# Performance work log

Hardware: AMD Instinct MI355X
Metric: run time of the kernel (lower is better)

## Reference

```python
import jax, jax.numpy as jnp
import numpy as np

N = 200_000
E = 6_400_000
EPS = 1e-12


def l2_normalize(x):
    # F.normalize(x, p=2, dim=1): x / max(||x||_2, eps)
    n = jnp.linalg.norm(x, axis=1, keepdims=True)
    return x / jnp.maximum(n, EPS)


def gcn_conv(x, W, b, src, dst, n):
    """PyG GCNConv: add self-loops, symmetric normalization D^-1/2 A D^-1/2,
    linear transform (no bias) on nodes, scatter-add to targets, then + bias."""
    loop = jnp.arange(n)
    s = jnp.concatenate([src, loop])  # sources (messages gathered here)
    d = jnp.concatenate([dst, loop])  # targets (aggregation here)
    deg = jax.ops.segment_sum(jnp.ones(s.shape[0], dtype=x.dtype), d, num_segments=n)
    dinv = jnp.where(deg > 0, jax.lax.rsqrt(deg), 0.0)
    norm = dinv[s] * dinv[d]  # [E+N]
    h = x @ W  # [N, out]
    out = jax.ops.segment_sum(norm[:, None] * h[s], d, num_segments=n)
    return out + b


def setup_inputs() -> dict:
    key = jax.random.key(0)
    ks = jax.random.split(key, 10)
    x = jax.random.normal(ks[0], (N, 3), dtype=jnp.float32)
    edge_index = jax.random.randint(ks[1], (2, E), 0, N, dtype=jnp.int64)

    def glorot(k, shape):
        lim = float(np.sqrt(6.0 / (shape[0] + shape[1])))
        return jax.random.uniform(k, shape, jnp.float32, -lim, lim)

    return {
        "x": x,
        "edge_index": edge_index,
        "W1": glorot(ks[2], (3, 6)),   "b1": jnp.zeros((6,), jnp.float32),
        "W2": glorot(ks[3], (6, 12)),  "b2": jnp.zeros((12,), jnp.float32),
        "W3": glorot(ks[4], (12, 24)), "b3": jnp.zeros((24,), jnp.float32),
        "Wc": glorot(ks[5], (24, 13)), "bc": jnp.zeros((13,), jnp.float32),
    }


def reference(x, edge_index, W1, b1, W2, b2, W3, b3, Wc, bc):
    src, dst = edge_index[0], edge_index[1]
    n = x.shape[0]
    h = jnp.tanh(gcn_conv(x, W1, b1, src, dst, n))
    h = jnp.tanh(l2_normalize(gcn_conv(h, W2, b2, src, dst, n)))
    h = l2_normalize(gcn_conv(h, W3, b3, src, dst, n))
    h = h @ Wc + bc
    return l2_normalize(h)
```

## Files before the change

### kernel.cpp

```cpp
#include <hip/hip_runtime.h>
#include <math.h>


static constexpr int NN = 200000;
static constexpr int NE = 6400000;
static constexpr int BK = 256;

static constexpr int SUBW  = 512;
static constexpr int NBA   = (NN + SUBW - 1) / SUBW;
static constexpr int CAP   = 32;
static constexpr int FLUSH = 16;
static constexpr int CAPB  = 18400;
static constexpr int BKP   = 512;
static constexpr int EPT   = 4;
static constexpr int CHUNK = BKP * EPT;
static constexpr int GPART = 768;
static constexpr int SRCSH = 13;
static constexpr int NSB   = (NN + (1 << SRCSH) - 1) >> SRCSH;

static constexpr int S     = 4;
static constexpr int LOGS  = 2;

__global__ void __launch_bounds__(BKP) k_part(const int* __restrict__ srcI,
                                              const int* __restrict__ dstI,
                                              unsigned* __restrict__ stg,
                                              int* __restrict__ gtail, int e) {
  __shared__ unsigned bin[CAP][NBA];
  __shared__ int bcnt[NBA];
  for (int t = threadIdx.x; t < NBA; t += BKP) bcnt[t] = 0;
  __syncthreads();
  int nchunks = (e + CHUNK - 1) / CHUNK;
  for (int c = blockIdx.x; c < nchunks; c += gridDim.x) {
    int base_i = c * CHUNK;
    int dv[EPT], sv[EPT];
#pragma unroll
    for (int u = 0; u < EPT; ++u) {
      int i = base_i + u * BKP + (int)threadIdx.x;
      dv[u] = (i < e) ? __builtin_nontemporal_load(dstI + i) : -1;
      sv[u] = (i < e) ? __builtin_nontemporal_load(srcI + i) : 0;
    }
#pragma unroll
    for (int u = 0; u < EPT; ++u) {
      if (dv[u] >= 0) {
        int b = dv[u] >> 9;
        unsigned rec = ((unsigned)(dv[u] & (SUBW - 1)) << 18) | (unsigned)sv[u];
        int p = atomicAdd(&bcnt[b], 1);
        if (p < CAP) {
          bin[p][b] = rec;
        } else {
          int base = atomicAdd(&gtail[b], 1);
          stg[(size_t)b * CAPB + base] = rec;
        }
      }
    }
    __syncthreads();
    int b2 = threadIdx.x;
    if (b2 < NBA) {
      int c2 = bcnt[b2];
      if (c2 > CAP) c2 = CAP;
      if (c2 >= FLUSH) {
        int nfl = c2 & ~(FLUSH - 1);
        int base = atomicAdd(&gtail[b2], nfl);
        size_t o = (size_t)b2 * CAPB + base;
        for (int k = 0; k < nfl; k += 4) {
          uint4 v;
          v.x = bin[k][b2]; v.y = bin[k + 1][b2]; v.z = bin[k + 2][b2]; v.w = bin[k + 3][b2];
          *(uint4*)(stg + o + k) = v;
        }
        int r = c2 - nfl;
        for (int k = 0; k < r; ++k) bin[k][b2] = bin[nfl + k][b2];
        bcnt[b2] = r;
      }
    }
    __syncthreads();
  }
  int b2 = threadIdx.x;
  if (b2 < NBA) {
    int c2 = bcnt[b2];
    if (c2 > CAP) c2 = CAP;
    if (c2 > 0) {
      int base = atomicAdd(&gtail[b2], c2);
      size_t o = (size_t)b2 * CAPB + base;
      for (int k = 0; k < c2; ++k) stg[o + k] = bin[k][b2];
    }
  }
}

__global__ void k_scan_sub(const int* __restrict__ gtail, int* __restrict__ sbase) {
  __shared__ int s0[512], s1[512];
  int t = threadIdx.x;
  int v = (t < NBA) ? gtail[t] : 0;
  s0[t] = v;
  __syncthreads();
  int* a = s0; int* b = s1;
  for (int off = 1; off < 512; off <<= 1) {
    int x = a[t] + ((t >= off) ? a[t - off] : 0);
    b[t] = x;
    __syncthreads();
    int* tmp = a; a = b; b = tmp;
  }
  if (t < NBA) sbase[t] = a[t] - v;
}

__global__ void __launch_bounds__(BK) k_build(const unsigned* __restrict__ stg,
                                              const int* __restrict__ gtail,
                                              const int* __restrict__ sbase,
                                              int* __restrict__ rowptr,
                                              int* __restrict__ adj) {
  __shared__ unsigned hist2[SUBW * NSB];
  __shared__ int htot[SUBW];
  __shared__ int s0[SUBW], s1[SUBW];
  int b = blockIdx.x;
  int m = gtail[b]; if (m > CAPB) m = CAPB;
  size_t off = (size_t)b * CAPB;
  int base = sbase[b];
  if (b == NBA - 1 && threadIdx.x == 0) rowptr[NN] = base + m;
  for (int t = threadIdx.x; t < SUBW * NSB; t += BK) hist2[t] = 0;
  __syncthreads();
  for (int k = threadIdx.x; k < m; k += BK) {
    unsigned rec = stg[off + k];
    int dl = rec >> 18;
    int sb = (int)((rec & 0x3FFFFu) >> SRCSH);
    atomicAdd(&hist2[dl * NSB + sb], 1u);
  }
  __syncthreads();
  for (int dl = threadIdx.x; dl < SUBW; dl += BK) {
    unsigned run = 0;
    for (int sb = 0; sb < NSB; ++sb) {
      unsigned c = hist2[dl * NSB + sb];
      hist2[dl * NSB + sb] = run;
      run += c;
    }
    htot[dl] = (int)run;
    s0[dl] = (int)run;
  }
  __syncthreads();
  int* a = s0; int* bb = s1;
  for (int o2 = 1; o2 < SUBW; o2 <<= 1) {
    for (int t = threadIdx.x; t < SUBW; t += BK) bb[t] = a[t] + ((t >= o2) ? a[t - o2] : 0);
    __syncthreads();
    int* tmp = a; a = bb; bb = tmp;
  }
  for (int t = threadIdx.x; t < SUBW; t += BK) {
    int node = b * SUBW + t;
    int ex = a[t] - htot[t];
    if (node < NN) rowptr[node] = base + ex;
    bb[t] = ex;
  }
  __syncthreads();
  for (int k = threadIdx.x; k < m; k += BK) {
    unsigned rec = stg[off + k];
    int dl = rec >> 18;
    unsigned src = rec & 0x3FFFFu;
    int sb = (int)(src >> SRCSH);
    int p = bb[dl] + (int)atomicAdd(&hist2[dl * NSB + sb], 1u);
    adj[base + p] = (int)src;
  }
}

__global__ void k_zero(int* __restrict__ p, int n) {
  int i = blockIdx.x * blockDim.x + threadIdx.x;
  if (i < n) p[i] = 0;
}

__global__ void k_dinv(const int* __restrict__ rowptr, float* __restrict__ dinv, int n) {
  int i = blockIdx.x * blockDim.x + threadIdx.x;
  if (i < n) dinv[i] = rsqrtf(1.0f + (float)(rowptr[i + 1] - rowptr[i]));
}

__global__ void k_prep(const float* __restrict__ x, const float* __restrict__ dinv,
                       float* __restrict__ p1, int n) {
  int i = blockIdx.x * blockDim.x + threadIdx.x;
  if (i >= n) return;
  float di = dinv[i];
  float3 v;
  v.x = di * x[3 * (size_t)i];
  v.y = di * x[3 * (size_t)i + 1];
  v.z = di * x[3 * (size_t)i + 2];
  *(float3*)(p1 + 3 * (size_t)i) = v;
}

template <int RW> struct RowT;
template <> struct RowT<3> {
  using T = float3;
  static __device__ inline T ld(const float* __restrict__ p) { return *(const float3*)p; }
  static __device__ inline void add(float* __restrict__ a, const T& v) {
    a[0] += v.x; a[1] += v.y; a[2] += v.z;
  }
};
template <> struct RowT<6> {
  struct T { float2 a, b, c; };
  static __device__ inline T ld(const float* __restrict__ p) {
    T t; t.a = *(const float2*)p; t.b = *(const float2*)(p + 2); t.c = *(const float2*)(p + 4);
    return t;
  }
  static __device__ inline void add(float* __restrict__ a, const T& v) {
    a[0] += v.a.x; a[1] += v.a.y; a[2] += v.b.x; a[3] += v.b.y; a[4] += v.c.x; a[5] += v.c.y;
  }
};
template <> struct RowT<12> {
  struct T { float4 a, b, c; };
  static __device__ inline T ld(const float* __restrict__ p) {
    T t; t.a = *(const float4*)p; t.b = *(const float4*)(p + 4); t.c = *(const float4*)(p + 8);
    return t;
  }
  static __device__ inline void add(float* __restrict__ a, const T& v) {
    a[0] += v.a.x; a[1] += v.a.y; a[2] += v.a.z; a[3] += v.a.w;
    a[4] += v.b.x; a[5] += v.b.y; a[6] += v.b.z; a[7] += v.b.w;
    a[8] += v.c.x; a[9] += v.c.y; a[10] += v.c.z; a[11] += v.c.w;
  }
};

template <int RW, int UN>
__device__ inline void gather_p(const int* __restrict__ adj, int st, int en,
                                const float* __restrict__ pin, float* __restrict__ acc,
                                int slot) {
  using RT = RowT<RW>;
  using T = typename RT::T;
  int k = st + slot;
  if (k + (UN - 1) * S < en) {
    int a[UN];
#pragma unroll
    for (int u = 0; u < UN; ++u) a[u] = adj[k + u * S];
    for (;;) {
      int kn = k + UN * S;
      bool more = (kn + (UN - 1) * S < en);
      int b[UN];
#pragma unroll
      for (int u = 0; u < UN; ++u) b[u] = 0;
      if (more) {
#pragma unroll
        for (int u = 0; u < UN; ++u) b[u] = adj[kn + u * S];
      }
      T v[UN];
#pragma unroll
      for (int u = 0; u < UN; ++u) v[u] = RT::ld(pin + (size_t)a[u] * RW);
#pragma unroll
      for (int u = 0; u < UN; ++u) RT::add(acc, v[u]);
      k = kn;
      if (!more) break;
#pragma unroll
      for (int u = 0; u < UN; ++u) a[u] = b[u];
    }
  }
  for (; k < en; k += S) {
    T v = RT::ld(pin + (size_t)adj[k] * RW);
    RT::add(acc, v);
  }
}

template <int FIN>
__device__ inline void group_reduce(float* __restrict__ acc) {
#pragma unroll
  for (int j = 0; j < FIN; ++j) {
    acc[j] += __shfl_xor(acc[j], 1);
    acc[j] += __shfl_xor(acc[j], 2);
  }
}

template <int RW, int FOUT, int MODE>
__global__ void __launch_bounds__(BK, 8) k_gather_fused(
    const int* __restrict__ adj, const int* __restrict__ rowptr,
    const float* __restrict__ pin, const float* __restrict__ W,
    const float* __restrict__ bias, const float* __restrict__ dinv,
    float* __restrict__ pout, int n) {
  __shared__ float sW[RW * FOUT];
  __shared__ float sb[FOUT];
  for (int t = threadIdx.x; t < RW * FOUT; t += BK) sW[t] = W[t];
  if (threadIdx.x < FOUT) sb[threadIdx.x] = bias[threadIdx.x];
  __syncthreads();
  int g = blockIdx.x * blockDim.x + threadIdx.x;
  int i = g >> LOGS;
  int slot = g & (S - 1);
  if (i >= n) return;
  float acc[RW] = {};
  if (slot == 0) {
    typename RowT<RW>::T v = RowT<RW>::ld(pin + (size_t)i * RW);
    RowT<RW>::add(acc, v);
  }
  gather_p<RW, 4>(adj, rowptr[i], rowptr[i + 1], pin, acc, slot);
  group_reduce<RW>(acc);
  float di = dinv[i];
  float h[FOUT];
  float ss = 0.f;
#pragma unroll
  for (int j = 0; j < FOUT; ++j) {
    float s = 0.f;
#pragma unroll
    for (int kk = 0; kk < RW; ++kk) s = fmaf(acc[kk], sW[kk * FOUT + j], s);
    float t = fmaf(di, s, sb[j]);
    h[j] = t;
    ss += t * t;
  }
  float o[FOUT];
  if (MODE == 0) {
#pragma unroll
    for (int j = 0; j < FOUT; ++j) o[j] = di * tanhf(h[j]);
  } else {
    float inv = 1.f / fmaxf(sqrtf(ss), 1e-12f);
#pragma unroll
    for (int j = 0; j < FOUT; ++j) o[j] = di * tanhf(h[j] * inv);
  }
  if (slot == 0) {
    float* po = pout + (size_t)i * FOUT;
    if (MODE == 0) {
      *(float2*)(po)     = make_float2(o[0], o[1]);
      *(float2*)(po + 2) = make_float2(o[2], o[3]);
      *(float2*)(po + 4) = make_float2(o[4], o[5]);
    } else {
      *(float4*)(po)     = make_float4(o[0], o[1], o[2], o[3]);
      *(float4*)(po + 4) = make_float4(o[4], o[5], o[6], o[7]);
      *(float4*)(po + 8) = make_float4(o[8], o[9], o[10], o[11]);
    }
  }
}

__global__ void __launch_bounds__(BK, 6) k_gather_final(
    const int* __restrict__ adj, const int* __restrict__ rowptr,
    const float* __restrict__ pin, const float* __restrict__ W3,
    const float* __restrict__ b3, const float* __restrict__ Wc,
    const float* __restrict__ bc, const float* __restrict__ dinv,
    float* __restrict__ out, int n) {
  constexpr int RW = 12, FOUT = 24, FC = 13;
  __shared__ float sW[RW * FOUT];
  __shared__ float sb[FOUT];
  __shared__ float sWc[FOUT * FC];
  __shared__ float sbc[FC];
  for (int t = threadIdx.x; t < RW * FOUT; t += BK) sW[t] = W3[t];
  for (int t = threadIdx.x; t < FOUT * FC; t += BK) sWc[t] = Wc[t];
  if (threadIdx.x < FOUT) sb[threadIdx.x] = b3[threadIdx.x];
  if (threadIdx.x < FC) sbc[threadIdx.x] = bc[threadIdx.x];
  __syncthreads();
  int g = blockIdx.x * blockDim.x + threadIdx.x;
  int i = g >> LOGS;
  int slot = g & (S - 1);
  if (i >= n) return;
  float acc[RW] = {};
  if (slot == 0) {
    RowT<RW>::T v = RowT<RW>::ld(pin + (size_t)i * RW);
    RowT<RW>::add(acc, v);
  }
  gather_p<RW, 4>(adj, rowptr[i], rowptr[i + 1], pin, acc, slot);
  group_reduce<RW>(acc);
  float di = dinv[i];
  float h[FOUT];
  float ss = 0.f;
#pragma unroll
  for (int j = 0; j < FOUT; ++j) {
    float s = 0.f;
#pragma unroll
    for (int kk = 0; kk < RW; ++kk) s = fmaf(acc[kk], sW[kk * FOUT + j], s);
    float t = fmaf(di, s, sb[j]);
    h[j] = t;
    ss += t * t;
  }
  float inv = 1.f / fmaxf(sqrtf(ss), 1e-12f);
  float v[FC];
  float ss2 = 0.f;
#pragma unroll
  for (int j = 0; j < FC; ++j) {
    float s = sbc[j];
#pragma unroll
    for (int kk = 0; kk < FOUT; ++kk) s = fmaf(h[kk] * inv, sWc[kk * FC + j], s);
    v[j] = s;
    ss2 += s * s;
  }
  float inv2 = 1.f / fmaxf(sqrtf(ss2), 1e-12f);
  if (slot == 0) {
#pragma unroll
    for (int j = 0; j < FC; ++j) out[(size_t)i * FC + j] = v[j] * inv2;
  }
}

extern "C" void kernel_launch(void* const* d_in, const int* in_sizes, int n_in,
                              void* d_out, int out_size, void* d_ws, size_t ws_size,
                              hipStream_t stream) {
  const float* x  = (const float*)d_in[0];
  const int*   ei = (const int*)d_in[1];
  const float* W1 = (const float*)d_in[2];
  const float* b1 = (const float*)d_in[3];
  const float* W2 = (const float*)d_in[4];
  const float* b2 = (const float*)d_in[5];
  const float* W3 = (const float*)d_in[6];
  const float* b3 = (const float*)d_in[7];
  const float* Wc = (const float*)d_in[8];
  const float* bc = (const float*)d_in[9];
  float* out = (float*)d_out;

  const int n = NN;
  const int e = NE;
  const int* srcI = ei;
  const int* dstI = ei + e;

  float* ws = (float*)d_ws;
  float* dinv  = ws;
  int* rowptr  = (int*)(ws + n);
  int* gtail   = rowptr + n + 8;
  int* sbase   = gtail + 512;
  int* adj     = sbase + 512;
  size_t roff = (size_t)n + (n + 8) + 512 + 512 + e;
  roff = (roff + 15) & ~(size_t)15;
  float* R     = ws + roff;
  unsigned* stg = (unsigned*)R;
  float* p1 = R;
  float* p2 = R + (size_t)3 * n;
  float* p3 = R + (size_t)9 * n;

  const int gn  = (n + BK - 1) / BK;
  const int gnS = (n * S + BK - 1) / BK;

  k_zero<<<2, BK, 0, stream>>>(gtail, 512);
  k_part<<<GPART, BKP, 0, stream>>>(srcI, dstI, stg, gtail, e);
  k_scan_sub<<<1, 512, 0, stream>>>(gtail, sbase);
  k_build<<<NBA, BK, 0, stream>>>(stg, gtail, sbase, rowptr, adj);
  k_dinv<<<gn, BK, 0, stream>>>(rowptr, dinv, n);

  k_prep<<<gn, BK, 0, stream>>>(x, dinv, p1, n);

  k_gather_fused<3, 6, 0><<<gnS, BK, 0, stream>>>(adj, rowptr, p1, W1, b1, dinv, p2, n);

  k_gather_fused<6, 12, 1><<<gnS, BK, 0, stream>>>(adj, rowptr, p2, W2, b2, dinv, p3, n);

  k_gather_final<<<gnS, BK, 0, stream>>>(adj, rowptr, p3, W3, b3, Wc, bc, dinv, out, n);
}
```

Baseline: 468.7 us.

## Split layer-2/3 gathers into source-range phases for cache locality

```diff
diff --git a/kernel.cpp b/kernel.cpp
--- a/kernel.cpp
+++ b/kernel.cpp
@@ -106,7 +106,10 @@
                                               const int* __restrict__ gtail,
                                               const int* __restrict__ sbase,
                                               int* __restrict__ rowptr,
-                                              int* __restrict__ adj) {
+                                              int* __restrict__ adj,
+                                              int* __restrict__ b7,
+                                              int* __restrict__ b13,
+                                              int* __restrict__ b19) {
   __shared__ unsigned hist2[SUBW * NSB];
   __shared__ int htot[SUBW];
   __shared__ int s0[SUBW], s1[SUBW];
@@ -144,7 +147,12 @@
   for (int t = threadIdx.x; t < SUBW; t += BK) {
     int node = b * SUBW + t;
     int ex = a[t] - htot[t];
-    if (node < NN) rowptr[node] = base + ex;
+    if (node < NN) {
+      rowptr[node] = base + ex;
+      b7[node]  = base + ex + (int)hist2[t * NSB + 7];
+      b13[node] = base + ex + (int)hist2[t * NSB + 13];
+      b19[node] = base + ex + (int)hist2[t * NSB + 19];
+    }
     bb[t] = ex;
   }
   __syncthreads();
@@ -187,6 +195,9 @@
   static __device__ inline void add(float* __restrict__ a, const T& v) {
     a[0] += v.x; a[1] += v.y; a[2] += v.z;
   }
+  static __device__ inline void st(float* __restrict__ p, const float* __restrict__ a) {
+    *(float3*)p = make_float3(a[0], a[1], a[2]);
+  }
 };
 template <> struct RowT<6> {
   struct T { float2 a, b, c; };
@@ -197,6 +208,11 @@
   static __device__ inline void add(float* __restrict__ a, const T& v) {
     a[0] += v.a.x; a[1] += v.a.y; a[2] += v.b.x; a[3] += v.b.y; a[4] += v.c.x; a[5] += v.c.y;
   }
+  static __device__ inline void st(float* __restrict__ p, const float* __restrict__ a) {
+    *(float2*)(p)     = make_float2(a[0], a[1]);
+    *(float2*)(p + 2) = make_float2(a[2], a[3]);
+    *(float2*)(p + 4) = make_float2(a[4], a[5]);
+  }
 };
 template <> struct RowT<12> {
   struct T { float4 a, b, c; };
@@ -208,6 +224,11 @@
     a[0] += v.a.x; a[1] += v.a.y; a[2] += v.a.z; a[3] += v.a.w;
     a[4] += v.b.x; a[5] += v.b.y; a[6] += v.b.z; a[7] += v.b.w;
     a[8] += v.c.x; a[9] += v.c.y; a[10] += v.c.z; a[11] += v.c.w;
+  }
+  static __device__ inline void st(float* __restrict__ p, const float* __restrict__ a) {
+    *(float4*)(p)     = make_float4(a[0], a[1], a[2], a[3]);
+    *(float4*)(p + 4) = make_float4(a[4], a[5], a[6], a[7]);
+    *(float4*)(p + 8) = make_float4(a[8], a[9], a[10], a[11]);
   }
 };
 
@@ -315,32 +336,60 @@
   }
 }
 
-__global__ void __launch_bounds__(BK, 6) k_gather_final(
-    const int* __restrict__ adj, const int* __restrict__ rowptr,
-    const float* __restrict__ pin, const float* __restrict__ W3,
-    const float* __restrict__ b3, const float* __restrict__ Wc,
-    const float* __restrict__ bc, const float* __restrict__ dinv,
-    float* __restrict__ out, int n) {
-  constexpr int RW = 12, FOUT = 24, FC = 13;
-  __shared__ float sW[RW * FOUT];
-  __shared__ float sb[FOUT];
-  __shared__ float sWc[FOUT * FC];
-  __shared__ float sbc[FC];
-  for (int t = threadIdx.x; t < RW * FOUT; t += BK) sW[t] = W3[t];
-  for (int t = threadIdx.x; t < FOUT * FC; t += BK) sWc[t] = Wc[t];
-  if (threadIdx.x < FOUT) sb[threadIdx.x] = b3[threadIdx.x];
-  if (threadIdx.x < FC) sbc[threadIdx.x] = bc[threadIdx.x];
-  __syncthreads();
+template <int RW, bool FIRST>
+__global__ void __launch_bounds__(BK, 8) k_gphase(
+    const int* __restrict__ adj, const int* __restrict__ stA,
+    const int* __restrict__ enB, const float* __restrict__ pin,
+    float* __restrict__ accb, int n) {
   int g = blockIdx.x * blockDim.x + threadIdx.x;
   int i = g >> LOGS;
   int slot = g & (S - 1);
   if (i >= n) return;
   float acc[RW] = {};
   if (slot == 0) {
-    RowT<RW>::T v = RowT<RW>::ld(pin + (size_t)i * RW);
+    if (FIRST) {
+      typename RowT<RW>::T v = RowT<RW>::ld(pin + (size_t)i * RW);
+      RowT<RW>::add(acc, v);
+    } else {
+      typename RowT<RW>::T v = RowT<RW>::ld(accb + (size_t)i * RW);
+      RowT<RW>::add(acc, v);
+    }
+  }
+  gather_p<RW, 2>(adj, stA[i], enB[i], pin, acc, slot);
+  group_reduce<RW>(acc);
+  if (slot == 0) RowT<RW>::st(accb + (size_t)i * RW, acc);
+}
+
+template <int RW, int FOUT, int MODE>
+__global__ void __launch_bounds__(BK, 6) k_gphase_last(
+    const int* __restrict__ adj, const int* __restrict__ stA,
+    const int* __restrict__ rowptr, const float* __restrict__ pin,
+    const float* __restrict__ W, const float* __restrict__ bias,
+    const float* __restrict__ Wc, const float* __restrict__ bc,
+    const float* __restrict__ dinv, const float* __restrict__ accb,
+    float* __restrict__ out, int n) {
+  constexpr int FC = 13;
+  __shared__ float sW[RW * FOUT];
+  __shared__ float sb[FOUT];
+  __shared__ float sWc[MODE == 2 ? FOUT * FC : 1];
+  __shared__ float sbc[MODE == 2 ? FC : 1];
+  for (int t = threadIdx.x; t < RW * FOUT; t += BK) sW[t] = W[t];
+  if (threadIdx.x < FOUT) sb[threadIdx.x] = bias[threadIdx.x];
+  if (MODE == 2) {
+    for (int t = threadIdx.x; t < FOUT * FC; t += BK) sWc[t] = Wc[t];
+    if (threadIdx.x < FC) sbc[threadIdx.x] = bc[threadIdx.x];
+  }
+  __syncthreads();
+  int g = blockIdx.x * blockDim.x + threadIdx.x;
+  int i = g >> LOGS;
+  int slot = g & (S - 1);
+  if (i >= n) return;
+  float acc[RW] = {};
+  if (slot == 0) {
+    typename RowT<RW>::T v = RowT<RW>::ld(accb + (size_t)i * RW);
     RowT<RW>::add(acc, v);
   }
-  gather_p<RW, 4>(adj, rowptr[i], rowptr[i + 1], pin, acc, slot);
+  gather_p<RW, 2>(adj, stA[i], rowptr[i + 1], pin, acc, slot);
   group_reduce<RW>(acc);
   float di = dinv[i];
   float h[FOUT];
@@ -355,20 +404,32 @@
     ss += t * t;
   }
   float inv = 1.f / fmaxf(sqrtf(ss), 1e-12f);
-  float v[FC];
-  float ss2 = 0.f;
-#pragma unroll
-  for (int j = 0; j < FC; ++j) {
-    float s = sbc[j];
-#pragma unroll
-    for (int kk = 0; kk < FOUT; ++kk) s = fmaf(h[kk] * inv, sWc[kk * FC + j], s);
-    v[j] = s;
-    ss2 += s * s;
-  }
-  float inv2 = 1.f / fmaxf(sqrtf(ss2), 1e-12f);
-  if (slot == 0) {
-#pragma unroll
-    for (int j = 0; j < FC; ++j) out[(size_t)i * FC + j] = v[j] * inv2;
+  if (MODE == 1) {
+    float o[FOUT];
+#pragma unroll
+    for (int j = 0; j < FOUT; ++j) o[j] = di * tanhf(h[j] * inv);
+    if (slot == 0) {
+      float* po = out + (size_t)i * FOUT;
+      *(float4*)(po)     = make_float4(o[0], o[1], o[2], o[3]);
+      *(float4*)(po + 4) = make_float4(o[4], o[5], o[6], o[7]);
+      *(float4*)(po + 8) = make_float4(o[8], o[9], o[10], o[11]);
+    }
+  } else {
+    float v[FC];
+    float ss2 = 0.f;
+#pragma unroll
+    for (int j = 0; j < FC; ++j) {
+      float s = sbc[j];
+#pragma unroll
+      for (int kk = 0; kk < FOUT; ++kk) s = fmaf(h[kk] * inv, sWc[kk * FC + j], s);
+      v[j] = s;
+      ss2 += s * s;
+    }
+    float inv2 = 1.f / fmaxf(sqrtf(ss2), 1e-12f);
+    if (slot == 0) {
+#pragma unroll
+      for (int j = 0; j < FC; ++j) out[(size_t)i * FC + j] = v[j] * inv2;
+    }
   }
 }
 
@@ -398,13 +459,17 @@
   int* gtail   = rowptr + n + 8;
   int* sbase   = gtail + 512;
   int* adj     = sbase + 512;
-  size_t roff = (size_t)n + (n + 8) + 512 + 512 + e;
+  int* b7      = adj + e;
+  int* b13     = b7 + n;
+  int* b19     = b13 + n;
+  size_t roff = (size_t)n + (n + 8) + 512 + 512 + e + 3 * (size_t)n;
   roff = (roff + 15) & ~(size_t)15;
   float* R     = ws + roff;
   unsigned* stg = (unsigned*)R;
-  float* p1 = R;
-  float* p2 = R + (size_t)3 * n;
-  float* p3 = R + (size_t)9 * n;
+  float* p1   = R;
+  float* p2   = R + (size_t)3 * n;
+  float* p3   = R + (size_t)9 * n;
+  float* accb = R + (size_t)21 * n;
 
   const int gn  = (n + BK - 1) / BK;
   const int gnS = (n * S + BK - 1) / BK;
@@ -412,14 +477,20 @@
   k_zero<<<2, BK, 0, stream>>>(gtail, 512);
   k_part<<<GPART, BKP, 0, stream>>>(srcI, dstI, stg, gtail, e);
   k_scan_sub<<<1, 512, 0, stream>>>(gtail, sbase);
-  k_build<<<NBA, BK, 0, stream>>>(stg, gtail, sbase, rowptr, adj);
+  k_build<<<NBA, BK, 0, stream>>>(stg, gtail, sbase, rowptr, adj, b7, b13, b19);
   k_dinv<<<gn, BK, 0, stream>>>(rowptr, dinv, n);
 
   k_prep<<<gn, BK, 0, stream>>>(x, dinv, p1, n);
 
   k_gather_fused<3, 6, 0><<<gnS, BK, 0, stream>>>(adj, rowptr, p1, W1, b1, dinv, p2, n);
 
-  k_gather_fused<6, 12, 1><<<gnS, BK, 0, stream>>>(adj, rowptr, p2, W2, b2, dinv, p3, n);
-
-  k_gather_final<<<gnS, BK, 0, stream>>>(adj, rowptr, p3, W3, b3, Wc, bc, dinv, out, n);
-}
+  k_gphase<6, true><<<gnS, BK, 0, stream>>>(adj, rowptr, b13, p2, accb, n);
+  k_gphase_last<6, 12, 1><<<gnS, BK, 0, stream>>>(adj, b13, rowptr, p2, W2, b2,
+                                                  Wc, bc, dinv, accb, p3, n);
+
+  k_gphase<12, true><<<gnS, BK, 0, stream>>>(adj, rowptr, b7, p3, accb, n);
+  k_gphase<12, false><<<gnS, BK, 0, stream>>>(adj, b7, b13, p3, accb, n);
+  k_gphase<12, false><<<gnS, BK, 0, stream>>>(adj, b13, b19, p3, accb, n);
+  k_gphase_last<12, 24, 2><<<gnS, BK, 0, stream>>>(adj, b19, rowptr, p3, W3, b3,
+                                                   Wc, bc, dinv, accb, out, n);
+}
```

New measurement: 461.0 us. About the same (-1.7%).
